# Kernel tuning notes

Hardware: AMD Instinct MI355X
Metric: run time of the kernel (lower is better)

The kernel has to match this reference:

```python
import jax, jax.numpy as jnp
import numpy as np

N, E = 50000, 800000
SD, VD = 128, 16        # node scalar / vector channels
ESD, EVD = 32, 1        # edge scalar / vector channels
LN_EPS = 1e-5
VN_EPS = 1e-8


def setup_inputs():
    key = jax.random.key(0)
    ks = jax.random.split(key, 24)
    g = lambda i, shape, scale=0.05: jax.random.normal(ks[i], shape, dtype=jnp.float32) * scale
    inp = dict(
        node_s=jax.random.normal(ks[0], (N, SD), dtype=jnp.float32),
        node_v=jax.random.normal(ks[1], (N, VD, 3), dtype=jnp.float32),
        edge_index=jax.random.randint(ks[2], (2, E), 0, N, dtype=jnp.int32),
        edge_s=jax.random.normal(ks[3], (E, ESD), dtype=jnp.float32),
        edge_v=jax.random.normal(ks[4], (E, EVD, 3), dtype=jnp.float32),
        # LayerNorm (scalar channel) params
        ln_g=jnp.ones((SD,), jnp.float32), ln_b=jnp.zeros((SD,), jnp.float32),
        # edge_gvp: (ESD,EVD) -> (SD,VD)
        wes=g(5, (SD, ESD)), bes=jnp.zeros((SD,), jnp.float32),
        wev=g(6, (VD * 3, EVD * 3)), bev=jnp.zeros((VD * 3,), jnp.float32),
        # node_gvp: (SD,VD) -> (SD,VD)
        wns=g(7, (SD, SD)), bns=jnp.zeros((SD,), jnp.float32),
        wnv=g(8, (VD * 3, VD * 3)), bnv=jnp.zeros((VD * 3,), jnp.float32),
        # residual linears
        wrs=g(9, (SD, SD)), brs=jnp.zeros((SD,), jnp.float32),
        wrv=g(10, (VD * 3, VD * 3)), brv=jnp.zeros((VD * 3,), jnp.float32),
    )
    return inp


def _gvp(s, v, ws, bs, wv, bv, vo, scalar_act=True):
    """GVP with activations=(silu, None), vector_gate=True (faithful to source:
    fc_v acts on flattened [vi*3] coords)."""
    s_out = s @ ws.T + bs
    if scalar_act:
        s_out = jax.nn.silu(s_out)
    v_flat = v.reshape(v.shape[0], -1)                    # [*, vi*3]
    v_out = (v_flat @ wv.T + bv).reshape(v.shape[0], vo, 3)
    gate = jax.nn.sigmoid(s_out[..., :vo])
    v_out = v_out * gate[..., None]
    return s_out, v_out


def reference(node_s, node_v, edge_index, edge_s, edge_v,
              ln_g, ln_b, wes, bes, wev, bev, wns, bns, wnv, bnv,
              wrs, brs, wrv, brv):
    n = node_s.shape[0]
    # --- GVP LayerNorm (norm_first) ---
    mu = jnp.mean(node_s, axis=-1, keepdims=True)
    var = jnp.mean(jnp.square(node_s - mu), axis=-1, keepdims=True)
    s_n = (node_s - mu) * jax.lax.rsqrt(var + LN_EPS) * ln_g + ln_b
    vn2 = jnp.sum(jnp.square(node_v), axis=-1, keepdims=True)      # [N,VD,1]
    vnorm = jnp.sqrt(jnp.mean(vn2, axis=-2, keepdims=True) + VN_EPS)  # [N,1,1]
    v_n = node_v / vnorm

    # --- edge GVP ---
    ec_s, ec_v = _gvp(edge_s, edge_v, wes, bes, wev, bev, VD)      # [E,SD],[E,VD,3]

    # --- scatter-mean over destination nodes (nodes w/o incoming stay zero) ---
    dst = edge_index[1]
    cnt = jax.ops.segment_sum(jnp.ones((dst.shape[0],), ec_s.dtype), dst, num_segments=n)
    denom = jnp.maximum(cnt, 1.0)
    agg_s = jax.ops.segment_sum(ec_s, dst, num_segments=n) / denom[:, None]
    agg_v = jax.ops.segment_sum(ec_v, dst, num_segments=n) / denom[:, None, None]

    # --- node GVP on (normalized + aggregated) ---
    out_s, out_v = _gvp(s_n + agg_s, v_n + agg_v, wns, bns, wnv, bnv, VD)

    # --- residual linears (on normalized inputs; dropout = identity in eval) ---
    res_s = s_n @ wrs.T + brs
    res_v = (v_n.reshape(n, -1) @ wrv.T + brv).reshape(n, VD, 3)
    return out_s + res_s, out_v + res_v
```

## Files before the change

kernel.cpp:

```cpp
#include <hip/hip_runtime.h>

__device__ __forceinline__ float sigmoidf_(float x){ return 1.f/(1.f+__expf(-x)); }

__global__ void hist_kernel(const int* __restrict__ dst, int* __restrict__ cnt, int E){
  int e = blockIdx.x*blockDim.x + threadIdx.x;
  if (e < E) atomicAdd(&cnt[dst[e]], 1);
}

__global__ __launch_bounds__(1024) void scan_kernel(const int* __restrict__ cnt,
                                                    int* __restrict__ off,
                                                    int* __restrict__ wptr, int N){
  __shared__ int part[1024];
  const int t = threadIdx.x;
  const int chunk = (N + 1023) / 1024;
  const int lo = min(t*chunk, N), hi = min(lo+chunk, N);
  int s = 0;
  for (int i = lo; i < hi; i++) s += cnt[i];
  part[t] = s;
  __syncthreads();
  for (int o = 1; o < 1024; o <<= 1){
    int v = (t >= o) ? part[t-o] : 0;
    __syncthreads();
    part[t] += v;
    __syncthreads();
  }
  int run = part[t] - s;
  for (int i = lo; i < hi; i++){
    int c = cnt[i];
    off[i] = run; wptr[i] = run;
    run += c;
  }
  if (t == 1023) off[N] = part[1023];
}

__global__ void scatter_kernel(const int* __restrict__ dst, int* __restrict__ wptr,
                               int* __restrict__ csr, int* __restrict__ node2, int E){
  int e = blockIdx.x*blockDim.x + threadIdx.x;
  if (e < E){
    int d = dst[e];
    int pos = atomicAdd(&wptr[d], 1);
    csr[pos] = e;
    node2[pos] = d;
  }
}

__global__ __launch_bounds__(256) void edge_agg2_kernel(
    const float* __restrict__ edge_s, const float* __restrict__ edge_v,
    const int* __restrict__ csr, const int* __restrict__ node2,
    const int* __restrict__ off,
    const float* __restrict__ wes, const float* __restrict__ bes,
    const float* __restrict__ wev, const float* __restrict__ bev,
    float* __restrict__ aggS, float* __restrict__ aggV, int E)
{
  __shared__ float shT[256*17];
  __shared__ int   shNid[256];
  __shared__ int   shRunStart[258];
  __shared__ int   shRunNode[257];
  __shared__ int   shWaveCnt[4];
  __shared__ int   shNumRuns, shActCnt;

  const int t  = threadIdx.x;
  const int wv = t >> 6, ln = t & 63;
  const int p0 = blockIdx.x * 256;
  const int p  = p0 + t;
  const bool act = (p < E);

  int e = 0, nid = -1;
  if (act){ e = csr[p]; nid = node2[p]; }

  float es[32];
  float ev0 = 0.f, ev1 = 0.f, ev2 = 0.f;
  if (act){
    #pragma unroll
    for (int k = 0; k < 32; k += 4){
      float4 u = *(const float4*)(edge_s + (size_t)e*32 + k);
      es[k]=u.x; es[k+1]=u.y; es[k+2]=u.z; es[k+3]=u.w;
    }
    const float* pv = edge_v + (size_t)e*3;
    ev0 = pv[0]; ev1 = pv[1]; ev2 = pv[2];
  } else {
    #pragma unroll
    for (int k = 0; k < 32; k++) es[k] = 0.f;
  }

  shNid[t] = nid;
  __syncthreads();
  const int prevN = (t == 0) ? -2 : shNid[t-1];
  const bool flag = act && (nid != prevN);
  const unsigned long long bal = __ballot(flag);
  if (ln == 0) shWaveCnt[wv] = __popcll(bal);
  __syncthreads();
  if (t == 0){
    int s = 0;
    #pragma unroll
    for (int k = 0; k < 4; k++){ int c = shWaveCnt[k]; shWaveCnt[k] = s; s += c; }
    shNumRuns = s;
    shActCnt  = min(E - p0, 256);
  }
  __syncthreads();
  const int numRuns = shNumRuns;
  if (flag){
    const int rid = shWaveCnt[wv] + __popcll(bal & ((1ull<<ln) - 1ull));
    shRunStart[rid] = t;
    shRunNode[rid]  = nid;
  }
  if (t == 0) shRunStart[numRuns] = shActCnt;
  __syncthreads();

#define REDUCE_STORE(BASE, STRIDE, CHBASE)                                    \
  for (int r = (t >> 4); r < numRuns; r += 16){                               \
    const int c  = t & 15;                                                    \
    const int s0 = shRunStart[r], s1 = shRunStart[r+1];                       \
    const int nd = shRunNode[r];                                              \
    float sum = 0.f;                                                          \
    for (int j = s0; j < s1; j++) sum += shT[j*17 + c];                       \
    if (r == 0 || r == numRuns-1){                                            \
      const int deg = off[nd+1] - off[nd];                                    \
      atomicAdd(BASE + (size_t)nd*STRIDE + (CHBASE) + c,                      \
                sum * (1.f/(float)deg));                                      \
    } else {                                                                  \
      BASE[(size_t)nd*STRIDE + (CHBASE) + c] = sum * (1.f/(float)(s1 - s0));  \
    }                                                                         \
  }

  float g16[16];
  for (int cb = 0; cb < 128; cb += 16){
    float acc[16];
    #pragma unroll
    for (int c = 0; c < 16; c++){
      float a = bes[cb+c];
      const float* wr = wes + (size_t)(cb+c)*32;
      #pragma unroll
      for (int k = 0; k < 32; k++) a += es[k]*wr[k];
      acc[c] = a * sigmoidf_(a);
    }
    if (cb == 0){
      #pragma unroll
      for (int c = 0; c < 16; c++) g16[c] = sigmoidf_(acc[c]);
    }
    __syncthreads();
    #pragma unroll
    for (int c = 0; c < 16; c += 4)
      *(float4*)&shT[t*17 + c] = make_float4(acc[c],acc[c+1],acc[c+2],acc[c+3]);
    __syncthreads();
    REDUCE_STORE(aggS, 128, cb)
  }

  #pragma unroll
  for (int vb = 0; vb < 48; vb += 16){
    float vo[16];
    #pragma unroll
    for (int cc = 0; cc < 16; cc++){
      const int c = vb + cc;
      vo[cc] = (bev[c] + wev[c*3]*ev0 + wev[c*3+1]*ev1 + wev[c*3+2]*ev2)
               * g16[c/3];
    }
    __syncthreads();
    #pragma unroll
    for (int c = 0; c < 16; c += 4)
      *(float4*)&shT[t*17 + c] = make_float4(vo[c],vo[c+1],vo[c+2],vo[c+3]);
    __syncthreads();
    REDUCE_STORE(aggV, 48, vb)
  }
#undef REDUCE_STORE
}

#define NS_RS 68
#define NS_GS 17

__global__ __launch_bounds__(512, 4) void node_kernel(
    const float* __restrict__ node_s, const float* __restrict__ node_v,
    const float* __restrict__ ln_g, const float* __restrict__ ln_b,
    const float* __restrict__ wns, const float* __restrict__ bns,
    const float* __restrict__ wnv, const float* __restrict__ bnv,
    const float* __restrict__ wrs, const float* __restrict__ brs,
    const float* __restrict__ wrv, const float* __restrict__ brv,
    const float* __restrict__ aggS, const float* __restrict__ aggV,
    float* __restrict__ out_s, float* __restrict__ out_v, int N)
{
  __shared__ float shX[64*NS_RS];
  __shared__ float shS[64*NS_RS];
  __shared__ float shP1[128], shP2[128];
  __shared__ float shGate[64*NS_GS];

  const int tid  = threadIdx.x;
  const int lane = tid & 63;
  const int wv   = __builtin_amdgcn_readfirstlane(tid >> 6);
  const int i0   = blockIdx.x * 64;
  const int node = i0 + lane;

  if (wv < 2){
    float s1 = 0.f, s2 = 0.f;
    if (node < N){
      const float4* p = (const float4*)(node_s + (size_t)node*128 + wv*64);
      #pragma unroll
      for (int q = 0; q < 16; q++){
        const float4 v = p[q];
        s1 += (v.x+v.y)+(v.z+v.w);
        s2 += (v.x*v.x+v.y*v.y)+(v.z*v.z+v.w*v.w);
      }
    }
    shP1[wv*64+lane] = s1;
    shP2[wv*64+lane] = s2;
  }
  __syncthreads();

  float acc1[16], acc2[16];
  #pragma unroll
  for (int j = 0; j < 16; j++){ acc1[j]=0.f; acc2[j]=0.f; }
  const int cb = wv*16;

  for (int half = 0; half < 2; half++){
    const int kb = half*64;
    {
      const int n  = tid >> 3;
      const int kk = (tid & 7)*8;
      const int gn = i0 + n;
      const float s1 = shP1[n] + shP1[64+n];
      const float s2 = shP2[n] + shP2[64+n];
      const float m  = s1 * (1.f/128.f);
      const float r  = rsqrtf(s2*(1.f/128.f) - m*m + 1e-5f);
      float4 x0 = make_float4(0.f,0.f,0.f,0.f), x1 = x0, a0 = x0, a1v = x0;
      if (gn < N){
        const float4* ps = (const float4*)(node_s + (size_t)gn*128 + kb + kk);
        x0 = ps[0]; x1 = ps[1];
        const float4* pa = (const float4*)(aggS + (size_t)gn*128 + kb + kk);
        a0 = pa[0]; a1v = pa[1];
      }
      const float4 g0 = *(const float4*)(ln_g + kb + kk);
      const float4 g1 = *(const float4*)(ln_g + kb + kk + 4);
      const float4 b0 = *(const float4*)(ln_b + kb + kk);
      const float4 b1 = *(const float4*)(ln_b + kb + kk + 4);
      const float sn0 = (x0.x-m)*r*g0.x + b0.x;
      const float sn1 = (x0.y-m)*r*g0.y + b0.y;
      const float sn2 = (x0.z-m)*r*g0.z + b0.z;
      const float sn3 = (x0.w-m)*r*g0.w + b0.w;
      const float sn4 = (x1.x-m)*r*g1.x + b1.x;
      const float sn5 = (x1.y-m)*r*g1.y + b1.y;
      const float sn6 = (x1.z-m)*r*g1.z + b1.z;
      const float sn7 = (x1.w-m)*r*g1.w + b1.w;
      float* pS = &shS[n*NS_RS + kk];
      float* pX = &shX[n*NS_RS + kk];
      ((float4*)pS)[0] = make_float4(sn0,sn1,sn2,sn3);
      ((float4*)pS)[1] = make_float4(sn4,sn5,sn6,sn7);
      ((float4*)pX)[0] = make_float4(sn0+a0.x, sn1+a0.y, sn2+a0.z, sn3+a0.w);
      ((float4*)pX)[1] = make_float4(sn4+a1v.x, sn5+a1v.y, sn6+a1v.z, sn7+a1v.w);
    }
    __syncthreads();

    for (int kc = 0; kc < 64; kc += 8){
      const float4 xa = ((const float4*)&shX[lane*NS_RS + kc])[0];
      const float4 xb = ((const float4*)&shX[lane*NS_RS + kc])[1];
      const float4 sa = ((const float4*)&shS[lane*NS_RS + kc])[0];
      const float4 sb = ((const float4*)&shS[lane*NS_RS + kc])[1];
      #pragma unroll
      for (int j = 0; j < 16; j++){
        const float* w1 = wns + (size_t)(cb+j)*128 + kb + kc;
        const float* w2 = wrs + (size_t)(cb+j)*128 + kb + kc;
        const float4 u0 = ((const float4*)w1)[0], u1 = ((const float4*)w1)[1];
        const float4 y0 = ((const float4*)w2)[0], y1 = ((const float4*)w2)[1];
        acc1[j] += (xa.x*u0.x + xa.y*u0.y + xa.z*u0.z + xa.w*u0.w)
                 + (xb.x*u1.x + xb.y*u1.y + xb.z*u1.z + xb.w*u1.w);
        acc2[j] += (sa.x*y0.x + sa.y*y0.y + sa.z*y0.z + sa.w*y0.w)
                 + (sb.x*y1.x + sb.y*y1.y + sb.z*y1.z + sb.w*y1.w);
      }
    }
    __syncthreads();
  }

  {
    float o[16];
    #pragma unroll
    for (int j = 0; j < 16; j++){
      const float aa = acc1[j] + bns[cb+j];
      const float so = aa * sigmoidf_(aa);
      if (wv == 0) shGate[lane*NS_GS + j] = sigmoidf_(so);
      o[j] = so + acc2[j] + brs[cb+j];
    }
    if (node < N){
      float4* po = (float4*)(out_s + (size_t)node*128 + cb);
      #pragma unroll
      for (int q = 0; q < 4; q++)
        po[q] = make_float4(o[4*q],o[4*q+1],o[4*q+2],o[4*q+3]);
    }
  }
  __syncthreads();

  {
    const int vb = wv*6;
    float sv[48];
    float s3 = 0.f;
    if (node < N){
      const float4* pv = (const float4*)(node_v + (size_t)node*48);
      #pragma unroll
      for (int q = 0; q < 12; q++){
        const float4 v = pv[q];
        sv[4*q]=v.x; sv[4*q+1]=v.y; sv[4*q+2]=v.z; sv[4*q+3]=v.w;
        s3 += (v.x*v.x+v.y*v.y)+(v.z*v.z+v.w*v.w);
      }
    } else {
      #pragma unroll
      for (int k = 0; k < 48; k++) sv[k]=0.f;
    }
    const float rvn = rsqrtf(s3*(1.f/16.f) + 1e-8f);
    #pragma unroll
    for (int k = 0; k < 48; k++) sv[k] *= rvn;

    float a1[6], a2[6];
    #pragma unroll
    for (int j = 0; j < 6; j++){ a1[j]=0.f; a2[j]=0.f; }

    #pragma unroll
    for (int kc = 0; kc < 48; kc += 8){
      float xv[8];
      if (node < N){
        const float4* pa = (const float4*)(aggV + (size_t)node*48 + kc);
        const float4 av0 = pa[0], av1 = pa[1];
        xv[0]=sv[kc]+av0.x;   xv[1]=sv[kc+1]+av0.y;
        xv[2]=sv[kc+2]+av0.z; xv[3]=sv[kc+3]+av0.w;
        xv[4]=sv[kc+4]+av1.x; xv[5]=sv[kc+5]+av1.y;
        xv[6]=sv[kc+6]+av1.z; xv[7]=sv[kc+7]+av1.w;
      } else {
        #pragma unroll
        for (int q = 0; q < 8; q++) xv[q] = 0.f;
      }
      #pragma unroll
      for (int j = 0; j < 6; j++){
        const float* w1 = wnv + (size_t)(vb+j)*48 + kc;
        const float* w2 = wrv + (size_t)(vb+j)*48 + kc;
        const float4 u0 = ((const float4*)w1)[0], u1 = ((const float4*)w1)[1];
        const float4 y0 = ((const float4*)w2)[0], y1 = ((const float4*)w2)[1];
        a1[j] += (xv[0]*u0.x + xv[1]*u0.y + xv[2]*u0.z + xv[3]*u0.w)
               + (xv[4]*u1.x + xv[5]*u1.y + xv[6]*u1.z + xv[7]*u1.w);
        a2[j] += (sv[kc]*y0.x + sv[kc+1]*y0.y + sv[kc+2]*y0.z + sv[kc+3]*y0.w)
               + (sv[kc+4]*y1.x + sv[kc+5]*y1.y + sv[kc+6]*y1.z + sv[kc+7]*y1.w);
      }
    }
    if (node < N){
      const float g0 = shGate[lane*NS_GS + 2*wv];
      const float g1 = shGate[lane*NS_GS + 2*wv + 1];
      float ov[6];
      #pragma unroll
      for (int j = 0; j < 6; j++){
        const float g = (j < 3) ? g0 : g1;
        ov[j] = (a1[j] + bnv[vb+j])*g + a2[j] + brv[vb+j];
      }
      float2* po = (float2*)(out_v + (size_t)node*48 + vb);
      po[0] = make_float2(ov[0], ov[1]);
      po[1] = make_float2(ov[2], ov[3]);
      po[2] = make_float2(ov[4], ov[5]);
    }
  }
}

extern "C" void kernel_launch(void* const* d_in, const int* in_sizes, int n_in,
                              void* d_out, int out_size, void* d_ws, size_t ws_size,
                              hipStream_t stream)
{
  const float* node_s = (const float*)d_in[0];
  const float* node_v = (const float*)d_in[1];
  const int*   eidx   = (const int*)  d_in[2];
  const float* edge_s = (const float*)d_in[3];
  const float* edge_v = (const float*)d_in[4];
  const float* ln_g   = (const float*)d_in[5];
  const float* ln_b   = (const float*)d_in[6];
  const float* wes    = (const float*)d_in[7];
  const float* bes    = (const float*)d_in[8];
  const float* wev    = (const float*)d_in[9];
  const float* bev    = (const float*)d_in[10];
  const float* wns    = (const float*)d_in[11];
  const float* bns    = (const float*)d_in[12];
  const float* wnv    = (const float*)d_in[13];
  const float* bnv    = (const float*)d_in[14];
  const float* wrs    = (const float*)d_in[15];
  const float* brs    = (const float*)d_in[16];
  const float* wrv    = (const float*)d_in[17];
  const float* brv    = (const float*)d_in[18];

  const int N = in_sizes[0] / 128;
  const int E = in_sizes[3] / 32;
  const int* dst = eidx + E;

  float* aggS = (float*)d_ws;
  float* aggV = aggS + (size_t)N*128;

  int* off   = (int*)d_out;
  int* wptr  = off + (N + 1);
  int* csr   = wptr + N;
  int* node2 = csr + E;

  hipMemsetAsync(wptr, 0, (size_t)N*sizeof(int), stream);
  hipMemsetAsync(aggS, 0, (size_t)N*176*sizeof(float), stream);
  hist_kernel<<<(E+255)/256, 256, 0, stream>>>(dst, wptr, E);
  scan_kernel<<<1, 1024, 0, stream>>>(wptr, off, wptr, N);
  scatter_kernel<<<(E+255)/256, 256, 0, stream>>>(dst, wptr, csr, node2, E);

  edge_agg2_kernel<<<(E+255)/256, 256, 0, stream>>>(edge_s, edge_v, csr, node2, off,
                                                    wes, bes, wev, bev,
                                                    aggS, aggV, E);

  float* out_s = (float*)d_out;
  float* out_v = out_s + (size_t)N*128;
  node_kernel<<<(N+63)/64, 512, 0, stream>>>(node_s, node_v, ln_g, ln_b,
                                             wns, bns, wnv, bnv,
                                             wrs, brs, wrv, brv,
                                             aggS, aggV, out_s, out_v, N);
}
```

Measured before the change: 777.8 us.

## Compute edge scalar GVP with split-bf16 MFMA instead of scalar FMA loops

The edge scalar projection (32->128 per edge) now runs on MFMA 16x16x32 bf16 instructions. Both the edge features and the weights are split into high and low bf16 parts, and three products (hi*hi, lo*hi, hi*lo) are accumulated to keep close to fp32 accuracy. Weights are staged once per block into padded shared memory, and each wave loads edge rows through the CSR indices held in shared memory. This replaces the per-thread 4096-FMA loop with matrix-core work, at the cost of extra shared memory, an occupancy hint of 3, and a small precision loss from dropping the lo*lo term.

Measured after the change: 716.5 us. 1.09x faster.

```diff
diff --git a/kernel.cpp b/kernel.cpp
--- a/kernel.cpp
+++ b/kernel.cpp
@@ -1,6 +1,20 @@
 #include <hip/hip_runtime.h>
 
+typedef __attribute__((ext_vector_type(8))) short short8v;
+typedef __attribute__((ext_vector_type(4))) float f32x4;
+
 __device__ __forceinline__ float sigmoidf_(float x){ return 1.f/(1.f+__expf(-x)); }
+
+__device__ __forceinline__ void cvt8_hilo(const float* f, short8v& h, short8v& l){
+  #pragma unroll
+  for (int i = 0; i < 8; i++){
+    const unsigned u = __builtin_bit_cast(unsigned, f[i]);
+    h[i] = (short)(u >> 16);
+    const float hf = __builtin_bit_cast(float, u & 0xFFFF0000u);
+    const float lf = f[i] - hf;
+    l[i] = (short)(__builtin_bit_cast(unsigned, lf) >> 16);
+  }
+}
 
 __global__ void hist_kernel(const int* __restrict__ dst, int* __restrict__ cnt, int E){
   int e = blockIdx.x*blockDim.x + threadIdx.x;
@@ -44,7 +58,8 @@
   }
 }
 
-__global__ __launch_bounds__(256) void edge_agg2_kernel(
+#define WES_PAD 40
+__global__ __launch_bounds__(256, 3) void edge_agg3_kernel(
     const float* __restrict__ edge_s, const float* __restrict__ edge_v,
     const int* __restrict__ csr, const int* __restrict__ node2,
     const int* __restrict__ off,
@@ -52,7 +67,10 @@
     const float* __restrict__ wev, const float* __restrict__ bev,
     float* __restrict__ aggS, float* __restrict__ aggV, int E)
 {
+  __shared__ short wesH[128*WES_PAD];
+  __shared__ short wesL[128*WES_PAD];
   __shared__ float shT[256*17];
+  __shared__ int   shE[256];
   __shared__ int   shNid[256];
   __shared__ int   shRunStart[258];
   __shared__ int   shRunNode[257];
@@ -61,28 +79,35 @@
 
   const int t  = threadIdx.x;
   const int wv = t >> 6, ln = t & 63;
+  const int r15 = ln & 15, g4 = ln >> 4;
   const int p0 = blockIdx.x * 256;
   const int p  = p0 + t;
   const bool act = (p < E);
 
-  int e = 0, nid = -1;
-  if (act){ e = csr[p]; nid = node2[p]; }
-
-  float es[32];
-  float ev0 = 0.f, ev1 = 0.f, ev2 = 0.f;
-  if (act){
-    #pragma unroll
-    for (int k = 0; k < 32; k += 4){
-      float4 u = *(const float4*)(edge_s + (size_t)e*32 + k);
-      es[k]=u.x; es[k+1]=u.y; es[k+2]=u.z; es[k+3]=u.w;
-    }
-    const float* pv = edge_v + (size_t)e*3;
-    ev0 = pv[0]; ev1 = pv[1]; ev2 = pv[2];
-  } else {
-    #pragma unroll
-    for (int k = 0; k < 32; k++) es[k] = 0.f;
-  }
-
+  {
+    const int row = t >> 1, col = (t & 1)*16;
+    const float* src = wes + row*32 + col;
+    float f0[8], f1[8];
+    #pragma unroll
+    for (int q = 0; q < 8; q += 4){
+      float4 u = *(const float4*)(src + q);
+      f0[q]=u.x; f0[q+1]=u.y; f0[q+2]=u.z; f0[q+3]=u.w;
+      float4 v = *(const float4*)(src + 8 + q);
+      f1[q]=v.x; f1[q+1]=v.y; f1[q+2]=v.z; f1[q+3]=v.w;
+    }
+    short8v h0, l0, h1, l1;
+    cvt8_hilo(f0, h0, l0);
+    cvt8_hilo(f1, h1, l1);
+    *(short8v*)&wesH[row*WES_PAD + col]     = h0;
+    *(short8v*)&wesH[row*WES_PAD + col + 8] = h1;
+    *(short8v*)&wesL[row*WES_PAD + col]     = l0;
+    *(short8v*)&wesL[row*WES_PAD + col + 8] = l1;
+  }
+
+  const int eSelf = csr[act ? p : (E-1)];
+  int nid = -1;
+  if (act) nid = node2[p];
+  shE[t] = eSelf;
   shNid[t] = nid;
   __syncthreads();
   const int prevN = (t == 0) ? -2 : shNid[t-1];
@@ -105,7 +130,27 @@
     shRunNode[rid]  = nid;
   }
   if (t == 0) shRunStart[numRuns] = shActCnt;
-  __syncthreads();
+
+  float ev0 = 0.f, ev1 = 0.f, ev2 = 0.f;
+  if (act){
+    const float* pv = edge_v + (size_t)eSelf*3;
+    ev0 = pv[0]; ev1 = pv[1]; ev2 = pv[2];
+  }
+  float bs[8];
+  #pragma unroll
+  for (int cb = 0; cb < 8; cb++) bs[cb] = bes[cb*16 + r15];
+
+  __syncthreads();
+
+  short8v aH[4], aL[4];
+  #pragma unroll
+  for (int mt = 0; mt < 4; mt++){
+    const int e_ = shE[wv*64 + mt*16 + r15];
+    const float* pa = edge_s + (size_t)e_*32 + g4*8;
+    float4 u0 = *(const float4*)pa, u1 = *(const float4*)(pa+4);
+    float f[8] = {u0.x,u0.y,u0.z,u0.w,u1.x,u1.y,u1.z,u1.w};
+    cvt8_hilo(f, aH[mt], aL[mt]);
+  }
 
 #define REDUCE_STORE(BASE, STRIDE, CHBASE)                                    \
   for (int r = (t >> 4); r < numRuns; r += 16){                               \
@@ -124,26 +169,39 @@
   }
 
   float g16[16];
-  for (int cb = 0; cb < 128; cb += 16){
-    float acc[16];
-    #pragma unroll
-    for (int c = 0; c < 16; c++){
-      float a = bes[cb+c];
-      const float* wr = wes + (size_t)(cb+c)*32;
-      #pragma unroll
-      for (int k = 0; k < 32; k++) a += es[k]*wr[k];
-      acc[c] = a * sigmoidf_(a);
-    }
+  for (int cb = 0; cb < 8; cb++){
+    const int baddr = (cb*16 + r15)*WES_PAD + g4*8;
+    const short8v bH = *(const short8v*)&wesH[baddr];
+    const short8v bL = *(const short8v*)&wesL[baddr];
+    f32x4 acc0 = {0.f,0.f,0.f,0.f}, acc1 = acc0, acc2 = acc0, acc3 = acc0;
+    acc0 = __builtin_amdgcn_mfma_f32_16x16x32_bf16(aH[0], bH, acc0, 0,0,0);
+    acc1 = __builtin_amdgcn_mfma_f32_16x16x32_bf16(aH[1], bH, acc1, 0,0,0);
+    acc2 = __builtin_amdgcn_mfma_f32_16x16x32_bf16(aH[2], bH, acc2, 0,0,0);
+    acc3 = __builtin_amdgcn_mfma_f32_16x16x32_bf16(aH[3], bH, acc3, 0,0,0);
+    acc0 = __builtin_amdgcn_mfma_f32_16x16x32_bf16(aL[0], bH, acc0, 0,0,0);
+    acc1 = __builtin_amdgcn_mfma_f32_16x16x32_bf16(aL[1], bH, acc1, 0,0,0);
+    acc2 = __builtin_amdgcn_mfma_f32_16x16x32_bf16(aL[2], bH, acc2, 0,0,0);
+    acc3 = __builtin_amdgcn_mfma_f32_16x16x32_bf16(aL[3], bH, acc3, 0,0,0);
+    acc0 = __builtin_amdgcn_mfma_f32_16x16x32_bf16(aH[0], bL, acc0, 0,0,0);
+    acc1 = __builtin_amdgcn_mfma_f32_16x16x32_bf16(aH[1], bL, acc1, 0,0,0);
+    acc2 = __builtin_amdgcn_mfma_f32_16x16x32_bf16(aH[2], bL, acc2, 0,0,0);
+    acc3 = __builtin_amdgcn_mfma_f32_16x16x32_bf16(aH[3], bL, acc3, 0,0,0);
+    __syncthreads();
+    const float bb = bs[cb];
+    #pragma unroll
+    for (int j = 0; j < 4; j++){
+      const int rbase = wv*64 + g4*4 + j;
+      float a0 = acc0[j] + bb; shT[(rbase     )*17 + r15] = a0 * sigmoidf_(a0);
+      float a1 = acc1[j] + bb; shT[(rbase + 16)*17 + r15] = a1 * sigmoidf_(a1);
+      float a2 = acc2[j] + bb; shT[(rbase + 32)*17 + r15] = a2 * sigmoidf_(a2);
+      float a3 = acc3[j] + bb; shT[(rbase + 48)*17 + r15] = a3 * sigmoidf_(a3);
+    }
+    __syncthreads();
     if (cb == 0){
       #pragma unroll
-      for (int c = 0; c < 16; c++) g16[c] = sigmoidf_(acc[c]);
-    }
-    __syncthreads();
-    #pragma unroll
-    for (int c = 0; c < 16; c += 4)
-      *(float4*)&shT[t*17 + c] = make_float4(acc[c],acc[c+1],acc[c+2],acc[c+3]);
-    __syncthreads();
-    REDUCE_STORE(aggS, 128, cb)
+      for (int c = 0; c < 16; c++) g16[c] = sigmoidf_(shT[t*17 + c]);
+    }
+    REDUCE_STORE(aggS, 128, cb*16)
   }
 
   #pragma unroll
@@ -395,7 +453,7 @@
   scan_kernel<<<1, 1024, 0, stream>>>(wptr, off, wptr, N);
   scatter_kernel<<<(E+255)/256, 256, 0, stream>>>(dst, wptr, csr, node2, E);
 
-  edge_agg2_kernel<<<(E+255)/256, 256, 0, stream>>>(edge_s, edge_v, csr, node2, off,
+  edge_agg3_kernel<<<(E+255)/256, 256, 0, stream>>>(edge_s, edge_v, csr, node2, off,
                                                     wes, bes, wev, bev,
                                                     aggS, aggV, E);
 
```
